# Kernel tuning notes

Measured on AMD Instinct MI355X. Metric: run time of the kernel, lower is better.

The kernel has to match this reference:

```python
import jax, jax.numpy as jnp
import numpy as np

B, N, E0, F_IN, H, EMB, VEC, DPI = 1024, 256, 2048, 6, 32, 32, 26, 512


def setup_inputs() -> dict:
    key = jax.random.key(0)
    ks = jax.random.split(key, 16)
    # fixed urban scene graph, shared by every batch element, with self-loops
    src0 = jax.random.randint(ks[0], (E0,), 0, N, dtype=jnp.int32)
    dst0 = jax.random.randint(ks[1], (E0,), 0, N, dtype=jnp.int32)
    loops = jnp.arange(N, dtype=jnp.int32)
    src = jnp.concatenate([src0, loops])
    dst = jnp.concatenate([dst0, loops])

    s = 0.05
    return {
        "graph_feats": jax.random.normal(ks[2], (B, N, F_IN), jnp.float32),
        "vector": jax.random.normal(ks[3], (B, VEC), jnp.float32),
        "src": src,
        "dst": dst,
        "W1": jax.random.normal(ks[4], (F_IN, H), jnp.float32) * s,
        "b1": jnp.zeros((H,), jnp.float32),
        "W2": jax.random.normal(ks[5], (H, H), jnp.float32) * s,
        "b2": jnp.zeros((H,), jnp.float32),
        "W3": jax.random.normal(ks[6], (H, H), jnp.float32) * s,
        "b3": jnp.zeros((H,), jnp.float32),
        "W_emb": jax.random.normal(ks[7], (H, EMB), jnp.float32) * s,
        "b_emb": jnp.zeros((EMB,), jnp.float32),
        "W_pi": jax.random.normal(ks[8], (VEC + EMB, DPI), jnp.float32) * s,
        "b_pi": jnp.zeros((DPI,), jnp.float32),
        "W_vf": jax.random.normal(ks[9], (VEC + EMB, DPI), jnp.float32) * s,
        "b_vf": jnp.zeros((DPI,), jnp.float32),
    }


def _edge_norm(src, dst, n_nodes):
    # DGL GraphConv norm='both': out_deg(src)^-1/2 * in_deg(dst)^-1/2
    ones = jnp.ones(src.shape[0], jnp.float32)
    deg_out = jax.ops.segment_sum(ones, src, num_segments=n_nodes)
    deg_in = jax.ops.segment_sum(ones, dst, num_segments=n_nodes)
    inv_o = jnp.where(deg_out > 0, deg_out ** -0.5, 0.0)
    inv_i = jnp.where(deg_in > 0, deg_in ** -0.5, 0.0)
    return inv_o[src] * inv_i[dst]  # [E]


def _gconv(h, src, dst, norm, W, b):
    # h: [B, N, F]; symmetric-normalized aggregation then linear (DGL GraphConv)
    msg = h[:, src, :] * norm[None, :, None]          # [B, E, F]
    agg = jnp.zeros_like(h).at[:, dst, :].add(msg)     # [B, N, F]
    return agg @ W + b


def reference(graph_feats, vector, src, dst, W1, b1, W2, b2, W3, b3,
              W_emb, b_emb, W_pi, b_pi, W_vf, b_vf):
    n_nodes = graph_feats.shape[1]
    norm = _edge_norm(src, dst, n_nodes)
    h = jax.nn.relu(_gconv(graph_feats, src, dst, norm, W1, b1))
    h = jax.nn.relu(_gconv(h, src, dst, norm, W2, b2))
    h = jax.nn.relu(_gconv(h, src, dst, norm, W3, b3))  # three_layers=True
    hg = jnp.mean(h, axis=1)                 # dgl.mean_nodes -> [B, H]
    emb = hg @ W_emb + b_emb                 # [B, EMB]
    comb = jnp.concatenate([vector[:, :26], emb], axis=1)  # [B, 58]
    pi = jax.nn.relu(comb @ W_pi + b_pi)
    vf = jax.nn.relu(comb @ W_vf + b_vf)
    return pi, vf
```

## Files before the change

### kernel.cpp

```cpp
#include <hip/hip_runtime.h>
#include <hip/hip_fp16.h>

#define B_    1024
#define N_    256
#define E_    2304
#define EPT_  9
#define FIN_  6
#define VEC_  26
#define STR_  36

__global__ __launch_bounds__(256) void fused_kernel(
    const float* __restrict__ gf,
    const float* __restrict__ vec,
    const int* __restrict__ src, const int* __restrict__ dst,
    const float* __restrict__ W1, const float* __restrict__ b1,
    const float* __restrict__ W2, const float* __restrict__ b2,
    const float* __restrict__ W3, const float* __restrict__ b3,
    const float* __restrict__ We, const float* __restrict__ be,
    const float* __restrict__ Wpi, const float* __restrict__ bpi,
    const float* __restrict__ Wvf, const float* __restrict__ bvf,
    float2* __restrict__ out)
{
    __shared__ __align__(16) float buf[N_ * STR_];
    __shared__ unsigned int packedE[E_];
    __shared__ float part[8 * 33];
    __shared__ float hgl[32];
    __shared__ float comb[VEC_ + 32];

    const int t = threadIdx.x;
    const int b = blockIdx.x;

    int*   deg_o  = (int*)buf;
    int*   deg_i  = (int*)buf + 256;
    int*   scan   = (int*)buf + 512;
    int*   cursor = (int*)buf + 768;
    int*   bcnt   = (int*)buf + 1024;
    int*   boff   = (int*)buf + 1088;
    int*   perm   = (int*)buf + 1152;
    float* inv_o  = buf + 1408;
    float* inv_i  = buf + 1664;

    deg_o[t] = 0; deg_i[t] = 0;
    if (t < 64) bcnt[t] = 0;
    __syncthreads();

    int sB[EPT_], dB[EPT_];
#pragma unroll
    for (int i = 0; i < EPT_; ++i) {
        int e = t + 256 * i;
        sB[i] = src[e]; dB[i] = dst[e];
    }
#pragma unroll
    for (int i = 0; i < EPT_; ++i) {
        atomicAdd(&deg_o[sB[i]], 1);
        atomicAdd(&deg_i[dB[i]], 1);
    }
    __syncthreads();

    const int dI = deg_i[t];
    {
        int dO = deg_o[t];
        inv_o[t] = dO > 0 ? rsqrtf((float)dO) : 0.f;
        inv_i[t] = dI > 0 ? rsqrtf((float)dI) : 0.f;
        scan[t] = dI;
    }
    __syncthreads();
    for (int off = 1; off < N_; off <<= 1) {
        int v = (t >= off) ? scan[t - off] : 0;
        __syncthreads();
        scan[t] += v;
        __syncthreads();
    }
    cursor[t] = scan[t] - dI;
    int dmy = dI > 63 ? 63 : dI;
    atomicAdd(&bcnt[dmy], 1);
    __syncthreads();
    if (t == 0) { int run = 0; for (int i = 0; i < 64; ++i) { boff[i] = run; run += bcnt[i]; } }
    __syncthreads();
    { int pos = atomicAdd(&boff[dmy], 1); perm[pos] = t; }
#pragma unroll
    for (int i = 0; i < EPT_; ++i) {
        int s = sB[i], d = dB[i];
        int pos = atomicAdd(&cursor[d], 1);
        float nrm = inv_o[s] * inv_i[d];
        unsigned short h = __half_as_ushort(__float2half(nrm));
        packedE[pos] = ((unsigned int)s << 16) | (unsigned int)h;
    }
    __syncthreads();

    const int node = perm[t];
    const int end  = scan[node];
    const int beg  = end - deg_i[node];
    __syncthreads();

    {
        const float* g = gf + (size_t)b * (N_ * FIN_);
        for (int i = t; i < N_ * 8; i += 256) {
            int n = i >> 3, k = i & 7;
            buf[n * STR_ + k] = (k < FIN_) ? g[n * FIN_ + k] : 0.f;
        }
    }
    __syncthreads();

    float o[32];

    {
        float a[8] = {0,0,0,0,0,0,0,0};
        for (int e = beg; e < end; ++e) {
            unsigned int u = packedE[e];
            float w = __half2float(__ushort_as_half((unsigned short)(u & 0xffffu)));
            const float4* hr = (const float4*)&buf[(u >> 16) * STR_];
            float4 c0 = hr[0], c1 = hr[1];
            a[0] += w * c0.x; a[1] += w * c0.y; a[2] += w * c0.z; a[3] += w * c0.w;
            a[4] += w * c1.x; a[5] += w * c1.y;
        }
#pragma unroll
        for (int j = 0; j < 32; ++j) o[j] = b1[j];
#pragma unroll
        for (int k = 0; k < FIN_; ++k) {
            float ak = a[k];
            const float* wr = &W1[k * 32];
#pragma unroll
            for (int j = 0; j < 32; ++j) o[j] += ak * wr[j];
        }
#pragma unroll
        for (int j = 0; j < 32; ++j) o[j] = fmaxf(o[j], 0.f);
    }
    __syncthreads();
    {
        float4* row = (float4*)&buf[node * STR_];
#pragma unroll
        for (int q = 0; q < 8; ++q) row[q] = make_float4(o[4*q], o[4*q+1], o[4*q+2], o[4*q+3]);
    }
    __syncthreads();

    for (int L = 0; L < 2; ++L) {
        float acc[32];
#pragma unroll
        for (int k = 0; k < 32; ++k) acc[k] = 0.f;
        for (int e = beg; e < end; ++e) {
            unsigned int u = packedE[e];
            float w = __half2float(__ushort_as_half((unsigned short)(u & 0xffffu)));
            const float4* hr = (const float4*)&buf[(u >> 16) * STR_];
#pragma unroll
            for (int q = 0; q < 8; ++q) {
                float4 c = hr[q];
                acc[4*q]   += w * c.x;
                acc[4*q+1] += w * c.y;
                acc[4*q+2] += w * c.z;
                acc[4*q+3] += w * c.w;
            }
        }
        const float* Wl = (L == 0) ? W2 : W3;
        const float* Bl = (L == 0) ? b2 : b3;
#pragma unroll
        for (int j = 0; j < 32; ++j) o[j] = Bl[j];
#pragma unroll 8
        for (int k = 0; k < 32; ++k) {
            float ak = acc[k];
            const float* wr = &Wl[k * 32];
#pragma unroll
            for (int j = 0; j < 32; ++j) o[j] += ak * wr[j];
        }
#pragma unroll
        for (int j = 0; j < 32; ++j) o[j] = fmaxf(o[j], 0.f);
        __syncthreads();
        {
            float4* row = (float4*)&buf[node * STR_];
#pragma unroll
            for (int q = 0; q < 8; ++q) row[q] = make_float4(o[4*q], o[4*q+1], o[4*q+2], o[4*q+3]);
        }
        __syncthreads();
    }

    {
        int j = t & 31, g = t >> 5;
        float s = 0.f;
        for (int i = 0; i < 32; ++i) s += buf[(g * 32 + i) * STR_ + j];
        part[g * 33 + j] = s;
    }
    __syncthreads();
    if (t < 32) {
        float sum = 0.f;
#pragma unroll
        for (int g = 0; g < 8; ++g) sum += part[g * 33 + t];
        hgl[t] = sum * (1.0f / 256.0f);
    }
    __syncthreads();

    if (t < 32) {
        float v = be[t];
#pragma unroll
        for (int j = 0; j < 32; ++j) v += hgl[j] * We[j * 32 + t];
        comb[VEC_ + t] = v;
    }
    if (t < VEC_) comb[t] = vec[b * VEC_ + t];
    __syncthreads();

    {
        float p0 = bpi[2 * t], p1 = bpi[2 * t + 1];
        float v0 = bvf[2 * t], v1 = bvf[2 * t + 1];
        const float2* Wp = (const float2*)Wpi;
        const float2* Wv = (const float2*)Wvf;
        for (int k = 0; k < VEC_ + 32; ++k) {
            float c = comb[k];
            float2 a = Wp[k * 256 + t];
            p0 += c * a.x; p1 += c * a.y;
            float2 d = Wv[k * 256 + t];
            v0 += c * d.x; v1 += c * d.y;
        }
        out[b * 256 + t]          = make_float2(fmaxf(p0, 0.f), fmaxf(p1, 0.f));
        out[262144 + b * 256 + t] = make_float2(fmaxf(v0, 0.f), fmaxf(v1, 0.f));
    }
}

extern "C" void kernel_launch(void* const* d_in, const int* in_sizes, int n_in,
                              void* d_out, int out_size, void* d_ws, size_t ws_size,
                              hipStream_t stream)
{
    fused_kernel<<<B_, 256, 0, stream>>>(
        (const float*)d_in[0], (const float*)d_in[1],
        (const int*)d_in[2], (const int*)d_in[3],
        (const float*)d_in[4], (const float*)d_in[5],
        (const float*)d_in[6], (const float*)d_in[7],
        (const float*)d_in[8], (const float*)d_in[9],
        (const float*)d_in[10], (const float*)d_in[11],
        (const float*)d_in[12], (const float*)d_in[13],
        (const float*)d_in[14], (const float*)d_in[15],
        (float2*)d_out);
}
```

Before: 139.9 us.

## Store node features in fp16 shared memory with packed half2 FMA aggregation

Node feature rows in shared memory move from fp32 to fp16 with a 40-half stride. Edge aggregation now accumulates in packed half2 FMAs, halving LDS traffic per gathered row and doubling arithmetic throughput. The block-wide Hillis-Steele degree scan and the serial bucket offset loop are replaced by wavefront shuffle scans, which removes many barriers. Accumulating the aggregation in half precision risks accuracy loss, and fp16 storage also cuts LDS footprint, which may raise occupancy.

```diff
diff --git a/kernel.cpp b/kernel.cpp
--- a/kernel.cpp
+++ b/kernel.cpp
@@ -7,7 +7,7 @@
 #define EPT_  9
 #define FIN_  6
 #define VEC_  26
-#define STR_  36
+#define HSTR_ 40
 
 __global__ __launch_bounds__(256) void fused_kernel(
     const float* __restrict__ gf,
@@ -21,24 +21,26 @@
     const float* __restrict__ Wvf, const float* __restrict__ bvf,
     float2* __restrict__ out)
 {
-    __shared__ __align__(16) float buf[N_ * STR_];
+    __shared__ __align__(16) __half hbuf[N_ * HSTR_];
     __shared__ unsigned int packedE[E_];
     __shared__ float part[8 * 33];
     __shared__ float hgl[32];
     __shared__ float comb[VEC_ + 32];
+    __shared__ int   wsum[4];
 
     const int t = threadIdx.x;
     const int b = blockIdx.x;
-
-    int*   deg_o  = (int*)buf;
-    int*   deg_i  = (int*)buf + 256;
-    int*   scan   = (int*)buf + 512;
-    int*   cursor = (int*)buf + 768;
-    int*   bcnt   = (int*)buf + 1024;
-    int*   boff   = (int*)buf + 1088;
-    int*   perm   = (int*)buf + 1152;
-    float* inv_o  = buf + 1408;
-    float* inv_i  = buf + 1664;
+    const int lane = t & 63, wv = t >> 6;
+
+    int*   deg_o  = (int*)hbuf;
+    int*   deg_i  = (int*)hbuf + 256;
+    int*   scanA  = (int*)hbuf + 512;
+    int*   cursor = (int*)hbuf + 768;
+    int*   perm   = (int*)hbuf + 1024;
+    float* inv_o  = (float*)hbuf + 1280;
+    float* inv_i  = (float*)hbuf + 1536;
+    int*   bcnt   = (int*)hbuf + 1792;
+    int*   boff   = (int*)hbuf + 1856;
 
     deg_o[t] = 0; deg_i[t] = 0;
     if (t < 64) bcnt[t] = 0;
@@ -46,15 +48,9 @@
 
     int sB[EPT_], dB[EPT_];
 #pragma unroll
-    for (int i = 0; i < EPT_; ++i) {
-        int e = t + 256 * i;
-        sB[i] = src[e]; dB[i] = dst[e];
-    }
-#pragma unroll
-    for (int i = 0; i < EPT_; ++i) {
-        atomicAdd(&deg_o[sB[i]], 1);
-        atomicAdd(&deg_i[dB[i]], 1);
-    }
+    for (int i = 0; i < EPT_; ++i) { int e = t + 256 * i; sB[i] = src[e]; dB[i] = dst[e]; }
+#pragma unroll
+    for (int i = 0; i < EPT_; ++i) { atomicAdd(&deg_o[sB[i]], 1); atomicAdd(&deg_i[dB[i]], 1); }
     __syncthreads();
 
     const int dI = deg_i[t];
@@ -62,34 +58,50 @@
         int dO = deg_o[t];
         inv_o[t] = dO > 0 ? rsqrtf((float)dO) : 0.f;
         inv_i[t] = dI > 0 ? rsqrtf((float)dI) : 0.f;
-        scan[t] = dI;
-    }
-    __syncthreads();
-    for (int off = 1; off < N_; off <<= 1) {
-        int v = (t >= off) ? scan[t - off] : 0;
-        __syncthreads();
-        scan[t] += v;
-        __syncthreads();
-    }
-    cursor[t] = scan[t] - dI;
-    int dmy = dI > 63 ? 63 : dI;
-    atomicAdd(&bcnt[dmy], 1);
-    __syncthreads();
-    if (t == 0) { int run = 0; for (int i = 0; i < 64; ++i) { boff[i] = run; run += bcnt[i]; } }
-    __syncthreads();
-    { int pos = atomicAdd(&boff[dmy], 1); perm[pos] = t; }
+    }
+    int x = dI;
+#pragma unroll
+    for (int d = 1; d < 64; d <<= 1) {
+        int y = __shfl_up(x, d, 64);
+        if (lane >= d) x += y;
+    }
+    if (lane == 63) wsum[wv] = x;
+    const int bucket = dI > 63 ? 63 : dI;
+    atomicAdd(&bcnt[bucket], 1);
+    __syncthreads();
+
+    {
+        int prefix = 0;
+#pragma unroll
+        for (int w = 0; w < 3; ++w) if (w < wv) prefix += wsum[w];
+        int incl = x + prefix;
+        scanA[t]  = incl;
+        cursor[t] = incl - dI;
+    }
+    if (t < 64) {
+        int c = bcnt[t], xx = c;
+#pragma unroll
+        for (int d = 1; d < 64; d <<= 1) {
+            int y = __shfl_up(xx, d, 64);
+            if (lane >= d) xx += y;
+        }
+        boff[t] = xx - c;
+    }
+    __syncthreads();
+
+    { int pos = atomicAdd(&boff[bucket], 1); perm[pos] = t; }
 #pragma unroll
     for (int i = 0; i < EPT_; ++i) {
-        int s = sB[i], d = dB[i];
-        int pos = atomicAdd(&cursor[d], 1);
-        float nrm = inv_o[s] * inv_i[d];
+        int s = sB[i], dd = dB[i];
+        int pos = atomicAdd(&cursor[dd], 1);
+        float nrm = inv_o[s] * inv_i[dd];
         unsigned short h = __half_as_ushort(__float2half(nrm));
         packedE[pos] = ((unsigned int)s << 16) | (unsigned int)h;
     }
     __syncthreads();
 
     const int node = perm[t];
-    const int end  = scan[node];
+    const int end  = scanA[node];
     const int beg  = end - deg_i[node];
     __syncthreads();
 
@@ -97,23 +109,28 @@
         const float* g = gf + (size_t)b * (N_ * FIN_);
         for (int i = t; i < N_ * 8; i += 256) {
             int n = i >> 3, k = i & 7;
-            buf[n * STR_ + k] = (k < FIN_) ? g[n * FIN_ + k] : 0.f;
-        }
-    }
-    __syncthreads();
-
+            hbuf[n * HSTR_ + k] = __float2half((k < FIN_) ? g[n * FIN_ + k] : 0.f);
+        }
+    }
+    __syncthreads();
+
+    const __half2 z2 = __float2half2_rn(0.f);
     float o[32];
 
     {
-        float a[8] = {0,0,0,0,0,0,0,0};
+        __half2 a2[4] = {z2, z2, z2, z2};
         for (int e = beg; e < end; ++e) {
             unsigned int u = packedE[e];
-            float w = __half2float(__ushort_as_half((unsigned short)(u & 0xffffu)));
-            const float4* hr = (const float4*)&buf[(u >> 16) * STR_];
-            float4 c0 = hr[0], c1 = hr[1];
-            a[0] += w * c0.x; a[1] += w * c0.y; a[2] += w * c0.z; a[3] += w * c0.w;
-            a[4] += w * c1.x; a[5] += w * c1.y;
-        }
+            __half2 w2 = __half2half2(__ushort_as_half((unsigned short)(u & 0xffffu)));
+            union { float4 f4; __half2 h2[4]; } r;
+            r.f4 = *(const float4*)&hbuf[(u >> 16) * HSTR_];
+#pragma unroll
+            for (int q = 0; q < 4; ++q) a2[q] = __hfma2(w2, r.h2[q], a2[q]);
+        }
+        float a[FIN_];
+#pragma unroll
+        for (int k = 0; k < FIN_; ++k)
+            a[k] = (k & 1) ? __high2float(a2[k >> 1]) : __low2float(a2[k >> 1]);
 #pragma unroll
         for (int j = 0; j < 32; ++j) o[j] = b1[j];
 #pragma unroll
@@ -128,28 +145,41 @@
     }
     __syncthreads();
     {
-        float4* row = (float4*)&buf[node * STR_];
-#pragma unroll
-        for (int q = 0; q < 8; ++q) row[q] = make_float4(o[4*q], o[4*q+1], o[4*q+2], o[4*q+3]);
+        union { float4 f4; __half2 h2[4]; } w;
+        float4* row = (float4*)&hbuf[node * HSTR_];
+#pragma unroll
+        for (int q = 0; q < 4; ++q) {
+#pragma unroll
+            for (int r = 0; r < 4; ++r)
+                w.h2[r] = __floats2half2_rn(o[8 * q + 2 * r], o[8 * q + 2 * r + 1]);
+            row[q] = w.f4;
+        }
     }
     __syncthreads();
 
     for (int L = 0; L < 2; ++L) {
-        float acc[32];
-#pragma unroll
-        for (int k = 0; k < 32; ++k) acc[k] = 0.f;
+        __half2 acc2[16];
+#pragma unroll
+        for (int j = 0; j < 16; ++j) acc2[j] = z2;
         for (int e = beg; e < end; ++e) {
             unsigned int u = packedE[e];
-            float w = __half2float(__ushort_as_half((unsigned short)(u & 0xffffu)));
-            const float4* hr = (const float4*)&buf[(u >> 16) * STR_];
-#pragma unroll
-            for (int q = 0; q < 8; ++q) {
-                float4 c = hr[q];
-                acc[4*q]   += w * c.x;
-                acc[4*q+1] += w * c.y;
-                acc[4*q+2] += w * c.z;
-                acc[4*q+3] += w * c.w;
+            __half2 w2 = __half2half2(__ushort_as_half((unsigned short)(u & 0xffffu)));
+            const float4* hr = (const float4*)&hbuf[(u >> 16) * HSTR_];
+            union { float4 f4; __half2 h2[4]; } r0, r1, r2, r3;
+            r0.f4 = hr[0]; r1.f4 = hr[1]; r2.f4 = hr[2]; r3.f4 = hr[3];
+#pragma unroll
+            for (int q = 0; q < 4; ++q) {
+                acc2[q]      = __hfma2(w2, r0.h2[q], acc2[q]);
+                acc2[4 + q]  = __hfma2(w2, r1.h2[q], acc2[4 + q]);
+                acc2[8 + q]  = __hfma2(w2, r2.h2[q], acc2[8 + q]);
+                acc2[12 + q] = __hfma2(w2, r3.h2[q], acc2[12 + q]);
             }
+        }
+        float a[32];
+#pragma unroll
+        for (int i = 0; i < 16; ++i) {
+            a[2 * i]     = __low2float(acc2[i]);
+            a[2 * i + 1] = __high2float(acc2[i]);
         }
         const float* Wl = (L == 0) ? W2 : W3;
         const float* Bl = (L == 0) ? b2 : b3;
@@ -157,7 +187,7 @@
         for (int j = 0; j < 32; ++j) o[j] = Bl[j];
 #pragma unroll 8
         for (int k = 0; k < 32; ++k) {
-            float ak = acc[k];
+            float ak = a[k];
             const float* wr = &Wl[k * 32];
 #pragma unroll
             for (int j = 0; j < 32; ++j) o[j] += ak * wr[j];
@@ -166,24 +196,31 @@
         for (int j = 0; j < 32; ++j) o[j] = fmaxf(o[j], 0.f);
         __syncthreads();
         {
-            float4* row = (float4*)&buf[node * STR_];
-#pragma unroll
-            for (int q = 0; q < 8; ++q) row[q] = make_float4(o[4*q], o[4*q+1], o[4*q+2], o[4*q+3]);
+            union { float4 f4; __half2 h2[4]; } w;
+            float4* row = (float4*)&hbuf[node * HSTR_];
+#pragma unroll
+            for (int q = 0; q < 4; ++q) {
+#pragma unroll
+                for (int r = 0; r < 4; ++r)
+                    w.h2[r] = __floats2half2_rn(o[8 * q + 2 * r], o[8 * q + 2 * r + 1]);
+                row[q] = w.f4;
+            }
         }
         __syncthreads();
     }
 
     {
-        int j = t & 31, g = t >> 5;
+        int j = t & 31, g8 = t >> 5;
         float s = 0.f;
-        for (int i = 0; i < 32; ++i) s += buf[(g * 32 + i) * STR_ + j];
-        part[g * 33 + j] = s;
+        for (int i = 0; i < 32; ++i)
+            s += __half2float(hbuf[(g8 * 32 + i) * HSTR_ + j]);
+        part[g8 * 33 + j] = s;
     }
     __syncthreads();
     if (t < 32) {
         float sum = 0.f;
 #pragma unroll
-        for (int g = 0; g < 8; ++g) sum += part[g * 33 + t];
+        for (int g8 = 0; g8 < 8; ++g8) sum += part[g8 * 33 + t];
         hgl[t] = sum * (1.0f / 256.0f);
     }
     __syncthreads();
```

Result: faster. 125.2 us (-10.5%).
